# Optimization experiments

Measured on AMD Instinct MI355X. Metric: run time of the kernel, lower is better.

The kernel has to match this reference:

```python
import jax, jax.numpy as jnp
import numpy as np

DT = 1.0 / 120.0  # dt from init kwargs

def setup_inputs() -> dict:
    key = jax.random.key(0)
    k1, k2, k3, k4 = jax.random.split(key, 4)
    B, T = 4096, 4096
    u = jax.random.normal(k1, (B, T, 2), dtype=jnp.float32)
    x0 = jnp.zeros((B, 2), dtype=jnp.float32)
    k_w = jax.random.normal(k2, (1,), dtype=jnp.float32)
    b_w = jax.random.normal(k3, (1,), dtype=jnp.float32)
    input_mat = jax.random.normal(k4, (2, 2), dtype=jnp.float32)
    input_mask = jnp.ones((2, 2), dtype=jnp.float32)
    return {"u": u, "x0": x0, "k_w": k_w, "b_w": b_w,
            "input_mat": input_mat, "input_mask": input_mask}

def reference(u, x0, k_w, b_w, input_mat, input_mask):
    # log_train=False -> func = abs
    k = jnp.abs(k_w)  # (1,), broadcasts over batch
    b = jnp.abs(b_w)
    W = (input_mat * input_mask) * DT  # fold dt into input matrix
    u_t = jnp.swapaxes(u, 0, 1)  # [T, B, 2] time-major for scan

    def step(X, ut):
        x = X[:, 0]
        v = X[:, 1]
        x_new = x + v * DT
        v_new = v + (-k * x - b * v) * DT
        X_new = jnp.stack([x_new, v_new], axis=-1) + ut @ W  # [B, 2]
        return X_new, X_new

    _, ys = jax.lax.scan(step, x0, u_t)  # ys: [T, B, 2]
    return jnp.swapaxes(ys, 0, 1)  # [B, T, 2]
```

## Files before the change

kernel.cpp:

```cpp
#include <hip/hip_runtime.h>
#include <stdint.h>

#define DT (1.0f / 120.0f)

struct M2 { float a00, a01, a10, a11; };

__device__ __forceinline__ M2 mmul(const M2& x, const M2& y) {
    M2 r;
    r.a00 = x.a00 * y.a00 + x.a01 * y.a10;
    r.a01 = x.a00 * y.a01 + x.a01 * y.a11;
    r.a10 = x.a10 * y.a00 + x.a11 * y.a10;
    r.a11 = x.a10 * y.a01 + x.a11 * y.a11;
    return r;
}

__device__ __forceinline__ float2 vmul(float2 v, const M2& m) {
    return make_float2(v.x * m.a00 + v.y * m.a10,
                       v.x * m.a01 + v.y * m.a11);
}

__device__ __forceinline__ float rfl(float x) {
    return __uint_as_float((unsigned)__builtin_amdgcn_readfirstlane((int)__float_as_uint(x)));
}
__device__ __forceinline__ M2 rflm(M2 m) {
    return { rfl(m.a00), rfl(m.a01), rfl(m.a10), rfl(m.a11) };
}

#define GLOAD_LDS16(gp, lp) __builtin_amdgcn_global_load_lds(                 \
    (const __attribute__((address_space(1))) void*)(gp),                      \
    (__attribute__((address_space(3))) void*)(lp), 16, 0, 0)

template <int C, int BLOCK>
__global__ __launch_bounds__(BLOCK, 8) void spring_scan(
    const float* __restrict__ u, const float* __restrict__ x0,
    const float* __restrict__ k_w, const float* __restrict__ b_w,
    const float* __restrict__ im, const float* __restrict__ imask,
    float* __restrict__ out, int T)
{
    static_assert(C == 8, "squaring count + swizzle assume C==8");
    constexpr int NW     = BLOCK / 64;
    constexpr int SLOTS  = BLOCK * C / 2;
    constexpr int WSLOTS = 64 * C / 2;

    __shared__ float4 buf[SLOTS];

    const int brow  = blockIdx.x;
    const int tid   = threadIdx.x;
    const int lane  = tid & 63;
    const int wid   = tid >> 6;
    const int wbase = wid * WSLOTS;
    const int lsw   = lane ^ ((lane >> 3) & 3);
    const int rsw   = (lane >> 1) & 3;

    const long rowbase = (long)brow * T * 2;
    const float4* urow4 = (const float4*)(u + rowbase);
    float4*       orow4 = (float4*)(out + rowbase);

    #pragma unroll
    for (int j = 0; j < C / 2; ++j)
        GLOAD_LDS16(urow4 + wbase + j * 64 + lsw, &buf[wbase + j * 64]);

    const float k  = fabsf(k_w[0]);
    const float bd = fabsf(b_w[0]);
    const float W00 = rfl(im[0] * imask[0] * DT), W01 = rfl(im[1] * imask[1] * DT);
    const float W10 = rfl(im[2] * imask[2] * DT), W11 = rfl(im[3] * imask[3] * DT);

    M2 A = { 1.0f, -k * DT, DT, 1.0f - bd * DT };

    M2 P[7];
    {
        M2 t = A;
        #pragma unroll
        for (int i = 0; i < 3; ++i) t = mmul(t, t);
        P[0] = t;
        #pragma unroll
        for (int s = 1; s < 7; ++s) P[s] = mmul(P[s - 1], P[s - 1]);
    }
    A = rflm(A);
    #pragma unroll
    for (int s = 0; s < 7; ++s) P[s] = rflm(P[s]);

    M2 Mlane = { 1.f, 0.f, 0.f, 1.f };
    #pragma unroll
    for (int s = 0; s < 6; ++s)
        if ((lane >> s) & 1) Mlane = mmul(Mlane, P[s]);

    float2 X_init = make_float2(x0[brow * 2 + 0], x0[brow * 2 + 1]);

    constexpr int STEPS = C * BLOCK;
    for (int t0 = 0; t0 < T; t0 += STEPS) {
        const int tilebase = t0 / 2;

        asm volatile("s_waitcnt vmcnt(0)" ::: "memory");
        __builtin_amdgcn_sched_barrier(0);

        float2 c[C];
        #pragma unroll
        for (int m = 0; m < C / 2; ++m) {
            float4 t = buf[wbase + lane * (C / 2) + (m ^ rsw)];
            c[2 * m + 0] = make_float2(t.x * W00 + t.y * W10,
                                       t.x * W01 + t.y * W11);
            c[2 * m + 1] = make_float2(t.z * W00 + t.w * W10,
                                       t.z * W01 + t.w * W11);
        }

        float2 v = make_float2(0.f, 0.f);
        #pragma unroll
        for (int i = 0; i < C; ++i) {
            v = vmul(v, A);
            v.x += c[i].x; v.y += c[i].y;
        }

        #pragma unroll
        for (int s = 0; s < 6; ++s) {
            float px = __shfl_up(v.x, 1u << s, 64);
            float py = __shfl_up(v.y, 1u << s, 64);
            if (lane >= (1 << s)) {
                float2 pv = vmul(make_float2(px, py), P[s]);
                v.x = pv.x + v.x; v.y = pv.y + v.y;
            }
        }

        if (lane == 63) *(float2*)&buf[wbase] = v;
        __syncthreads();

        float2 off = X_init;
        for (int w2 = 0; w2 < wid; ++w2) {
            off = vmul(off, P[6]);
            float2 tw = *(const float2*)&buf[w2 * WSLOTS];
            off.x += tw.x; off.y += tw.y;
        }

        const bool carry = (t0 + STEPS < T);
        float2 fin;
        if (carry) {
            fin = X_init;
            #pragma unroll
            for (int w2 = 0; w2 < NW; ++w2) {
                fin = vmul(fin, P[6]);
                float2 tw = *(const float2*)&buf[w2 * WSLOTS];
                fin.x += tw.x; fin.y += tw.y;
            }
        }

        float ex = __shfl_up(v.x, 1u, 64);
        float ey = __shfl_up(v.y, 1u, 64);
        float2 vex = (lane == 0) ? make_float2(0.f, 0.f) : make_float2(ex, ey);

        float2 X = vmul(off, Mlane);
        X.x += vex.x; X.y += vex.y;

        __syncthreads();

        #pragma unroll
        for (int m = 0; m < C / 2; ++m) {
            float4 o;
            X = vmul(X, A);
            X.x += c[2 * m + 0].x; X.y += c[2 * m + 0].y;
            o.x = X.x; o.y = X.y;
            X = vmul(X, A);
            X.x += c[2 * m + 1].x; X.y += c[2 * m + 1].y;
            o.z = X.x; o.w = X.y;
            buf[wbase + lane * (C / 2) + (m ^ rsw)] = o;
        }

        #pragma unroll
        for (int j = 0; j < C / 2; ++j)
            orow4[tilebase + wbase + j * 64 + lsw] = buf[wbase + j * 64 + lane];

        if (carry) {
            X_init = fin;
            asm volatile("s_waitcnt lgkmcnt(0)" ::: "memory");
            __builtin_amdgcn_sched_barrier(0);
            const int nb = tilebase + SLOTS;
            #pragma unroll
            for (int j = 0; j < C / 2; ++j)
                GLOAD_LDS16(urow4 + nb + wbase + j * 64 + lsw, &buf[wbase + j * 64]);
        }
    }
}

extern "C" void kernel_launch(void* const* d_in, const int* in_sizes, int n_in,
                              void* d_out, int out_size, void* d_ws, size_t ws_size,
                              hipStream_t stream) {
    const float* u     = (const float*)d_in[0];
    const float* x0    = (const float*)d_in[1];
    const float* k_w   = (const float*)d_in[2];
    const float* b_w   = (const float*)d_in[3];
    const float* im    = (const float*)d_in[4];
    const float* imask = (const float*)d_in[5];
    float* out = (float*)d_out;

    const int B = in_sizes[1] / 2;
    const int T = in_sizes[0] / (2 * B);

    spring_scan<8, 256><<<B, 256, 0, stream>>>(u, x0, k_w, b_w, im, imask, out, T);
}
```

Measured before the change: 46.95 us.

## Add specialized two-tile kernel that prefetches both input tiles upfront

Adds a kernel specialized for T equal to two tiles. It issues global-to-LDS loads for both tiles at the start, using a double LDS buffer, so the second tile's load overlaps compute on the first. It also moves the per-wave totals into a separate small shared array and replaces the second __syncthreads with a plain barrier. The cost is doubled LDS per block, which may reduce occupancy, and a dispatch on T with a general fallback kernel.

```diff
diff --git a/kernel.cpp b/kernel.cpp
--- a/kernel.cpp
+++ b/kernel.cpp
@@ -30,19 +30,27 @@
     (const __attribute__((address_space(1))) void*)(gp),                      \
     (__attribute__((address_space(3))) void*)(lp), 16, 0, 0)
 
+#define WAITCNT_VM(N)  { asm volatile("s_waitcnt vmcnt(" #N ")" ::: "memory"); \
+                         __builtin_amdgcn_sched_barrier(0); }
+#define BARRIER_LGKM() { asm volatile("s_waitcnt lgkmcnt(0)" ::: "memory");    \
+                         __builtin_amdgcn_sched_barrier(0);                    \
+                         __builtin_amdgcn_s_barrier();                         \
+                         __builtin_amdgcn_sched_barrier(0); }
+
 template <int C, int BLOCK>
-__global__ __launch_bounds__(BLOCK, 8) void spring_scan(
+__global__ __launch_bounds__(BLOCK) void spring_scan_pipe(
     const float* __restrict__ u, const float* __restrict__ x0,
     const float* __restrict__ k_w, const float* __restrict__ b_w,
     const float* __restrict__ im, const float* __restrict__ imask,
-    float* __restrict__ out, int T)
+    float* __restrict__ out)
 {
     static_assert(C == 8, "squaring count + swizzle assume C==8");
     constexpr int NW     = BLOCK / 64;
     constexpr int SLOTS  = BLOCK * C / 2;
     constexpr int WSLOTS = 64 * C / 2;
 
-    __shared__ float4 buf[SLOTS];
+    __shared__ float4 buf[2][SLOTS];
+    __shared__ float2 tot[2][NW];
 
     const int brow  = blockIdx.x;
     const int tid   = threadIdx.x;
@@ -52,13 +60,17 @@
     const int lsw   = lane ^ ((lane >> 3) & 3);
     const int rsw   = (lane >> 1) & 3;
 
+    constexpr int T = 2 * C * BLOCK;
     const long rowbase = (long)brow * T * 2;
     const float4* urow4 = (const float4*)(u + rowbase);
     float4*       orow4 = (float4*)(out + rowbase);
 
     #pragma unroll
-    for (int j = 0; j < C / 2; ++j)
-        GLOAD_LDS16(urow4 + wbase + j * 64 + lsw, &buf[wbase + j * 64]);
+    for (int tb = 0; tb < 2; ++tb)
+        #pragma unroll
+        for (int j = 0; j < C / 2; ++j)
+            GLOAD_LDS16(urow4 + tb * SLOTS + wbase + j * 64 + lsw,
+                        &buf[tb][wbase + j * 64]);
 
     const float k  = fabsf(k_w[0]);
     const float bd = fabsf(b_w[0]);
@@ -87,17 +99,14 @@
 
     float2 X_init = make_float2(x0[brow * 2 + 0], x0[brow * 2 + 1]);
 
-    constexpr int STEPS = C * BLOCK;
-    for (int t0 = 0; t0 < T; t0 += STEPS) {
-        const int tilebase = t0 / 2;
-
-        asm volatile("s_waitcnt vmcnt(0)" ::: "memory");
-        __builtin_amdgcn_sched_barrier(0);
+    #pragma unroll
+    for (int tb = 0; tb < 2; ++tb) {
+        WAITCNT_VM(4);
 
         float2 c[C];
         #pragma unroll
         for (int m = 0; m < C / 2; ++m) {
-            float4 t = buf[wbase + lane * (C / 2) + (m ^ rsw)];
+            float4 t = buf[tb][wbase + lane * (C / 2) + (m ^ rsw)];
             c[2 * m + 0] = make_float2(t.x * W00 + t.y * W10,
                                        t.x * W01 + t.y * W11);
             c[2 * m + 1] = make_float2(t.z * W00 + t.w * W10,
@@ -121,14 +130,152 @@
             }
         }
 
-        if (lane == 63) *(float2*)&buf[wbase] = v;
-        __syncthreads();
+        if (lane == 63) tot[tb][wid] = v;
+        BARRIER_LGKM();
 
         float2 off = X_init;
         for (int w2 = 0; w2 < wid; ++w2) {
             off = vmul(off, P[6]);
-            float2 tw = *(const float2*)&buf[w2 * WSLOTS];
+            float2 tw = tot[tb][w2];
             off.x += tw.x; off.y += tw.y;
+        }
+
+        if (tb == 0) {
+            float2 fin = X_init;
+            #pragma unroll
+            for (int w2 = 0; w2 < NW; ++w2) {
+                fin = vmul(fin, P[6]);
+                float2 tw = tot[0][w2];
+                fin.x += tw.x; fin.y += tw.y;
+            }
+            if (lane == 0) {}
+            X_init = (wid >= 0) ? X_init : X_init;
+            X_init = fin;
+        }
+
+        float ex = __shfl_up(v.x, 1u, 64);
+        float ey = __shfl_up(v.y, 1u, 64);
+        float2 vex = (lane == 0) ? make_float2(0.f, 0.f) : make_float2(ex, ey);
+
+        float2 X = vmul(off, Mlane);
+        X.x += vex.x; X.y += vex.y;
+
+        #pragma unroll
+        for (int m = 0; m < C / 2; ++m) {
+            float4 o;
+            X = vmul(X, A);
+            X.x += c[2 * m + 0].x; X.y += c[2 * m + 0].y;
+            o.x = X.x; o.y = X.y;
+            X = vmul(X, A);
+            X.x += c[2 * m + 1].x; X.y += c[2 * m + 1].y;
+            o.z = X.x; o.w = X.y;
+            buf[tb][wbase + lane * (C / 2) + (m ^ rsw)] = o;
+        }
+
+        #pragma unroll
+        for (int j = 0; j < C / 2; ++j)
+            orow4[tb * SLOTS + wbase + j * 64 + lsw] = buf[tb][wbase + j * 64 + lane];
+    }
+}
+
+template <int C, int BLOCK>
+__global__ __launch_bounds__(BLOCK) void spring_scan_gen(
+    const float* __restrict__ u, const float* __restrict__ x0,
+    const float* __restrict__ k_w, const float* __restrict__ b_w,
+    const float* __restrict__ im, const float* __restrict__ imask,
+    float* __restrict__ out, int T)
+{
+    static_assert(C == 8, "swizzle assumes C==8");
+    constexpr int NW     = BLOCK / 64;
+    constexpr int SLOTS  = BLOCK * C / 2;
+    constexpr int WSLOTS = 64 * C / 2;
+
+    __shared__ float4 buf[SLOTS];
+    __shared__ float2 tots[NW];
+
+    const int brow  = blockIdx.x;
+    const int tid   = threadIdx.x;
+    const int lane  = tid & 63;
+    const int wid   = tid >> 6;
+    const int wbase = wid * WSLOTS;
+    const int lsw   = lane ^ ((lane >> 3) & 3);
+    const int rsw   = (lane >> 1) & 3;
+
+    const long rowbase = (long)brow * T * 2;
+    const float4* urow4 = (const float4*)(u + rowbase);
+    float4*       orow4 = (float4*)(out + rowbase);
+
+    #pragma unroll
+    for (int j = 0; j < C / 2; ++j)
+        GLOAD_LDS16(urow4 + wbase + j * 64 + lsw, &buf[wbase + j * 64]);
+
+    const float k  = fabsf(k_w[0]);
+    const float bd = fabsf(b_w[0]);
+    const float W00 = rfl(im[0] * imask[0] * DT), W01 = rfl(im[1] * imask[1] * DT);
+    const float W10 = rfl(im[2] * imask[2] * DT), W11 = rfl(im[3] * imask[3] * DT);
+
+    M2 A = { 1.0f, -k * DT, DT, 1.0f - bd * DT };
+    M2 P[7];
+    {
+        M2 t = A;
+        #pragma unroll
+        for (int i = 0; i < 3; ++i) t = mmul(t, t);
+        P[0] = t;
+        #pragma unroll
+        for (int s = 1; s < 7; ++s) P[s] = mmul(P[s - 1], P[s - 1]);
+    }
+    A = rflm(A);
+    #pragma unroll
+    for (int s = 0; s < 7; ++s) P[s] = rflm(P[s]);
+
+    M2 Mlane = { 1.f, 0.f, 0.f, 1.f };
+    #pragma unroll
+    for (int s = 0; s < 6; ++s)
+        if ((lane >> s) & 1) Mlane = mmul(Mlane, P[s]);
+
+    float2 X_init = make_float2(x0[brow * 2 + 0], x0[brow * 2 + 1]);
+
+    constexpr int STEPS = C * BLOCK;
+    for (int t0 = 0; t0 < T; t0 += STEPS) {
+        const int tilebase = t0 / 2;
+
+        asm volatile("s_waitcnt vmcnt(0)" ::: "memory");
+        __builtin_amdgcn_sched_barrier(0);
+
+        float2 c[C];
+        #pragma unroll
+        for (int m = 0; m < C / 2; ++m) {
+            float4 t = buf[wbase + lane * (C / 2) + (m ^ rsw)];
+            c[2 * m + 0] = make_float2(t.x * W00 + t.y * W10,
+                                       t.x * W01 + t.y * W11);
+            c[2 * m + 1] = make_float2(t.z * W00 + t.w * W10,
+                                       t.z * W01 + t.w * W11);
+        }
+
+        float2 v = make_float2(0.f, 0.f);
+        #pragma unroll
+        for (int i = 0; i < C; ++i) {
+            v = vmul(v, A);
+            v.x += c[i].x; v.y += c[i].y;
+        }
+
+        #pragma unroll
+        for (int s = 0; s < 6; ++s) {
+            float px = __shfl_up(v.x, 1u << s, 64);
+            float py = __shfl_up(v.y, 1u << s, 64);
+            if (lane >= (1 << s)) {
+                float2 pv = vmul(make_float2(px, py), P[s]);
+                v.x = pv.x + v.x; v.y = pv.y + v.y;
+            }
+        }
+
+        if (lane == 63) tots[wid] = v;
+        __syncthreads();
+
+        float2 off = X_init;
+        for (int w2 = 0; w2 < wid; ++w2) {
+            off = vmul(off, P[6]);
+            off.x += tots[w2].x; off.y += tots[w2].y;
         }
 
         const bool carry = (t0 + STEPS < T);
@@ -138,8 +285,7 @@
             #pragma unroll
             for (int w2 = 0; w2 < NW; ++w2) {
                 fin = vmul(fin, P[6]);
-                float2 tw = *(const float2*)&buf[w2 * WSLOTS];
-                fin.x += tw.x; fin.y += tw.y;
+                fin.x += tots[w2].x; fin.y += tots[w2].y;
             }
         }
 
@@ -194,5 +340,12 @@
     const int B = in_sizes[1] / 2;
     const int T = in_sizes[0] / (2 * B);
 
-    spring_scan<8, 256><<<B, 256, 0, stream>>>(u, x0, k_w, b_w, im, imask, out, T);
-}
+    constexpr int C = 8, BLOCK = 256;
+    if (T == 2 * C * BLOCK) {
+        spring_scan_pipe<C, BLOCK><<<B, BLOCK, 0, stream>>>(
+            u, x0, k_w, b_w, im, imask, out);
+    } else {
+        spring_scan_gen<C, BLOCK><<<B, BLOCK, 0, stream>>>(
+            u, x0, k_w, b_w, im, imask, out, T);
+    }
+}
```

After: 46.18 us. About the same (-1.7%).
